# Kernel optimization log

Hardware: AMD Instinct MI355X
Metric: run time of the kernel (lower is better)

The kernel has to match this reference:

```python
import jax, jax.numpy as jnp
import numpy as np

B, D_IN, D_OUT, N_SUBNET, G = 16384, 512, 512, 8, 2


def setup_inputs() -> dict:
    key = jax.random.key(0)
    k_x, k_g, k_w = jax.random.split(key, 3)
    x = jax.random.normal(k_x, (B, D_IN), dtype=jnp.float32)
    groups = jax.random.randint(k_g, (B, G), 0, N_SUBNET, dtype=jnp.int32)
    # per-expert Dense params (the 'subnets')
    W = jax.random.normal(k_w, (N_SUBNET, D_IN, D_OUT), dtype=jnp.float32) * (1.0 / np.sqrt(D_IN))
    b = jnp.zeros((N_SUBNET, D_OUT), dtype=jnp.float32)
    return {"x": x, "groups": groups, "W": W, "b": b}


def reference(x, groups, W, b):
    """SubnetGate: one-hot gated dispatch to per-group subnets + combine.

    Faithful math: gates = one_hot(groups[:, group_col], n_subnet);
    out = sum_e gates[:, e] * subnet_e(x). Since gates are one-hot the
    combine selects exactly one expert output per row (gate weight 1.0).
    """
    group_col = 0
    n_subnet = W.shape[0]
    idx_group = groups[:, group_col]                     # [B]
    gates = jax.nn.one_hot(idx_group, n_subnet, dtype=x.dtype)  # [B, E]
    # run every expert on the full batch (dense reference for the
    # gather-compute-scatter kernel), then gate-combine
    expert_out = jnp.einsum("bi,eio->beo", x, W) + b[None, :, :]  # [B, E, O]
    out = jnp.einsum("be,beo->bo", gates, expert_out)             # [B, O]
    return out
```

## Files before the change

### kernel.cpp

```cpp
#include <hip/hip_runtime.h>
#include <hip/hip_bf16.h>


#define NROWS   16384
#define KDIM    512
#define NDIM    512
#define NEXP    8
#define BM      128
#define BN      128
#define BK      64
#define NT_PER  4
#define KT_PER  8
#define TILE_ELEMS (BN * BK)
#define WS_ROWLIST_OFF 4096
#define WS_WT_OFF      (4096 + NEXP * NROWS * 4)

typedef __bf16        bf16x8 __attribute__((ext_vector_type(8)));
typedef float         f32x4  __attribute__((ext_vector_type(4)));
typedef unsigned int  u32x4  __attribute__((ext_vector_type(4)));

__device__ __forceinline__ unsigned int f2bf_u(float f) {
    unsigned int u = __builtin_bit_cast(unsigned int, f);
    return (u + 0x7FFFu + ((u >> 16) & 1u)) >> 16;
}

__device__ __forceinline__ void gl_lds16(const void* g, void* l) {
    __builtin_amdgcn_global_load_lds(
        (const __attribute__((address_space(1))) unsigned int*)g,
        (__attribute__((address_space(3))) unsigned int*)l, 16, 0, 0);
}

__global__ void zero_kernel(int* __restrict__ gcnt) {
    if (threadIdx.x < NEXP) gcnt[threadIdx.x] = 0;
}

__global__ void prep_kernel(const float* __restrict__ W,
                            const int* __restrict__ groups,
                            int* __restrict__ gcnt,
                            int* __restrict__ rowlist,
                            unsigned short* __restrict__ Wtile) {
    __shared__ __align__(16) unsigned short tl[TILE_ELEMS];
    __shared__ int lcnt[NEXP];
    __shared__ int lbase[NEXP];
    const int bid = blockIdx.x;
    const int tid = threadIdx.x;

    if (bid < 256) {
        const int e  = bid >> 5;
        const int nt = (bid >> 3) & 3;
        const int kt = bid & 7;
        const float* Wb = W + (size_t)e * (KDIM * NDIM);
        #pragma unroll
        for (int i = 0; i < 4; ++i) {
            int f = i * 256 + tid;
            int n = f & 127;
            int g = f >> 7;
            int col = nt * BN + n;
            unsigned int p[4];
            #pragma unroll
            for (int jj = 0; jj < 4; ++jj) {
                int k0 = kt * BK + g * 8 + jj * 2;
                unsigned int lo = f2bf_u(Wb[(size_t)k0 * NDIM + col]);
                unsigned int hi = f2bf_u(Wb[(size_t)(k0 + 1) * NDIM + col]);
                p[jj] = lo | (hi << 16);
            }
            *(u32x4*)&tl[n * 64 + (g ^ (n & 7)) * 8] = *(const u32x4*)p;
        }
        __syncthreads();
        unsigned short* dst = Wtile + (size_t)bid * TILE_ELEMS;
        #pragma unroll
        for (int i = 0; i < 4; ++i) {
            int off = (i * 256 + tid) * 8;
            *(u32x4*)&dst[off] = *(const u32x4*)&tl[off];
        }
    } else {
        const int base = (bid - 256) * 256;
        if (tid < NEXP) lcnt[tid] = 0;
        __syncthreads();
        int r = base + tid;
        int e = groups[r * 2];
        int pos = atomicAdd(&lcnt[e], 1);
        __syncthreads();
        if (tid < NEXP) lbase[tid] = atomicAdd(&gcnt[tid], lcnt[tid]);
        __syncthreads();
        rowlist[e * NROWS + lbase[e] + pos] = r;
    }
}

__global__ __launch_bounds__(256, 2)
void gemm_kernel(const float* __restrict__ x,
                 const int* __restrict__ counts,
                 const int* __restrict__ rowlist,
                 const unsigned short* __restrict__ Wtile,
                 const float* __restrict__ bias,
                 float* __restrict__ out) {
    __shared__ __align__(16) unsigned short Asm[BM * 72];
    __shared__ __align__(16) unsigned short Bsm[TILE_ELEMS];

    const int bid = blockIdx.x;
    const int e   = bid >> 9;
    const int mt  = (bid >> 2) & 127;
    const int nt  = bid & 3;
    const int cnt = counts[e];
    const int rb  = mt * BM;
    if (rb >= cnt) return;
    int m_valid = cnt - rb;
    if (m_valid > BM) m_valid = BM;
    const int* rl = rowlist + e * NROWS + rb;

    const int tid = threadIdx.x;
    const int w   = tid >> 6;
    const int ln  = tid & 63;
    const int q   = ln >> 4;
    const int l15 = ln & 15;
    const int wm  = (w >> 1) * 64;
    const int wn  = (w & 1) * 64;

    const float* srcp[4];
    #pragma unroll
    for (int i = 0; i < 4; ++i) {
        int f = i * 256 + tid;
        int m = f >> 3;
        int g = f & 7;
        srcp[i] = (m < m_valid) ? (x + (size_t)rl[m] * KDIM + g * 8) : nullptr;
    }

    const unsigned short* wt =
        Wtile + (size_t)((e * NT_PER + nt) * KT_PER) * TILE_ELEMS;

    f32x4 acc[4][4];
    #pragma unroll
    for (int mi = 0; mi < 4; ++mi)
        #pragma unroll
        for (int ni = 0; ni < 4; ++ni)
            acc[mi][ni] = (f32x4){0.f, 0.f, 0.f, 0.f};

    for (int kt = 0; kt < KT_PER; ++kt) {
        const unsigned short* wsrc = wt + (size_t)kt * TILE_ELEMS;
        #pragma unroll
        for (int i = 0; i < 4; ++i) {
            int off = (i * 256 + tid) * 8;
            gl_lds16(wsrc + off, &Bsm[off]);
        }
        #pragma unroll
        for (int i = 0; i < 4; ++i) {
            int f = i * 256 + tid;
            int m = f >> 3;
            int g = f & 7;
            u32x4 pack = {0u, 0u, 0u, 0u};
            if (srcp[i]) {
                const float* s = srcp[i] + kt * BK;
                f32x4 f0 = *(const f32x4*)s;
                f32x4 f1 = *(const f32x4*)(s + 4);
                pack.x = f2bf_u(f0.x) | (f2bf_u(f0.y) << 16);
                pack.y = f2bf_u(f0.z) | (f2bf_u(f0.w) << 16);
                pack.z = f2bf_u(f1.x) | (f2bf_u(f1.y) << 16);
                pack.w = f2bf_u(f1.z) | (f2bf_u(f1.w) << 16);
            }
            *(u32x4*)&Asm[m * 72 + g * 8] = pack;
        }
        __syncthreads();
        #pragma unroll
        for (int ks = 0; ks < 2; ++ks) {
            const int g = ks * 4 + q;
            bf16x8 af[4], bf[4];
            #pragma unroll
            for (int mi = 0; mi < 4; ++mi)
                af[mi] = *(const bf16x8*)&Asm[(wm + mi * 16 + l15) * 72 + g * 8];
            #pragma unroll
            for (int ni = 0; ni < 4; ++ni) {
                int n = wn + ni * 16 + l15;
                bf[ni] = *(const bf16x8*)&Bsm[n * 64 + (g ^ (n & 7)) * 8];
            }
            #pragma unroll
            for (int mi = 0; mi < 4; ++mi)
                #pragma unroll
                for (int ni = 0; ni < 4; ++ni)
                    acc[mi][ni] = __builtin_amdgcn_mfma_f32_16x16x32_bf16(
                        af[mi], bf[ni], acc[mi][ni], 0, 0, 0);
        }
        __syncthreads();
    }

    int growv[16];
    #pragma unroll
    for (int mi = 0; mi < 4; ++mi)
        #pragma unroll
        for (int r = 0; r < 4; ++r) {
            int rloc = wm + mi * 16 + q * 4 + r;
            growv[mi * 4 + r] = (rloc < m_valid) ? rl[rloc] : -1;
        }
    const int ncol0 = nt * BN + wn;
    #pragma unroll
    for (int ni = 0; ni < 4; ++ni) {
        int col = ncol0 + ni * 16 + l15;
        float bv = bias[e * NDIM + col];
        #pragma unroll
        for (int mi = 0; mi < 4; ++mi)
            #pragma unroll
            for (int r = 0; r < 4; ++r) {
                int gr = growv[mi * 4 + r];
                if (gr >= 0) out[(size_t)gr * NDIM + col] = acc[mi][ni][r] + bv;
            }
    }
}

extern "C" void kernel_launch(void* const* d_in, const int* in_sizes, int n_in,
                              void* d_out, int out_size, void* d_ws, size_t ws_size,
                              hipStream_t stream) {
    const float* x      = (const float*)d_in[0];
    const int*   groups = (const int*)d_in[1];
    const float* W      = (const float*)d_in[2];
    const float* b      = (const float*)d_in[3];
    float*       out    = (float*)d_out;

    char* ws = (char*)d_ws;
    int*            counts  = (int*)ws;
    int*            rowlist = (int*)(ws + WS_ROWLIST_OFF);
    unsigned short* Wtile   = (unsigned short*)(ws + WS_WT_OFF);

    zero_kernel<<<1, 64, 0, stream>>>(counts);
    prep_kernel<<<320, 256, 0, stream>>>(W, groups, counts, rowlist, Wtile);
    gemm_kernel<<<4096, 256, 0, stream>>>(x, counts, rowlist, Wtile, b, out);
}
```

Before: 122.5 us.

## Restructure grouped GEMM with register-direct A, double-buffered B, smaller M tile

The GEMM kernel now loads activations straight from global memory into registers in MFMA fragment layout, dropping the A shared-memory stage. It double-buffers the weight tile in LDS with prefetch of the next K slice, and halves BM to 64 so each wave owns 16 rows. Occupancy rises to 4 blocks per CU, blocks are interleaved across experts, and output writes use nontemporal stores. The weight prep is split over 4x more blocks, and the zero kernel is replaced with a memset. The trade-off is that weight tiles are reused across fewer rows, and the register-direct A loads are less coalesced.

After: 128.2 us. 4.6% more time.

```diff
diff --git a/kernel.cpp b/kernel.cpp
--- a/kernel.cpp
+++ b/kernel.cpp
@@ -6,7 +6,7 @@
 #define KDIM    512
 #define NDIM    512
 #define NEXP    8
-#define BM      128
+#define BM      64
 #define BN      128
 #define BK      64
 #define NT_PER  4
@@ -30,8 +30,13 @@
         (__attribute__((address_space(3))) unsigned int*)l, 16, 0, 0);
 }
 
-__global__ void zero_kernel(int* __restrict__ gcnt) {
-    if (threadIdx.x < NEXP) gcnt[threadIdx.x] = 0;
+__device__ __forceinline__ bf16x8 pack_bf8(f32x4 lo, f32x4 hi) {
+    u32x4 w;
+    w.x = f2bf_u(lo.x) | (f2bf_u(lo.y) << 16);
+    w.y = f2bf_u(lo.z) | (f2bf_u(lo.w) << 16);
+    w.z = f2bf_u(hi.x) | (f2bf_u(hi.y) << 16);
+    w.w = f2bf_u(hi.z) | (f2bf_u(hi.w) << 16);
+    return __builtin_bit_cast(bf16x8, w);
 }
 
 __global__ void prep_kernel(const float* __restrict__ W,
@@ -39,46 +44,42 @@
                             int* __restrict__ gcnt,
                             int* __restrict__ rowlist,
                             unsigned short* __restrict__ Wtile) {
-    __shared__ __align__(16) unsigned short tl[TILE_ELEMS];
+    __shared__ __align__(16) unsigned short tl4[32 * 64];
     __shared__ int lcnt[NEXP];
     __shared__ int lbase[NEXP];
     const int bid = blockIdx.x;
     const int tid = threadIdx.x;
 
-    if (bid < 256) {
-        const int e  = bid >> 5;
-        const int nt = (bid >> 3) & 3;
-        const int kt = bid & 7;
+    if (bid < 1024) {
+        const int tile = bid >> 2;
+        const int qq   = bid & 3;
+        const int e  = tile >> 5;
+        const int nt = (tile >> 3) & 3;
+        const int kt = tile & 7;
         const float* Wb = W + (size_t)e * (KDIM * NDIM);
-        #pragma unroll
-        for (int i = 0; i < 4; ++i) {
-            int f = i * 256 + tid;
-            int n = f & 127;
-            int g = f >> 7;
-            int col = nt * BN + n;
-            unsigned int p[4];
-            #pragma unroll
-            for (int jj = 0; jj < 4; ++jj) {
-                int k0 = kt * BK + g * 8 + jj * 2;
-                unsigned int lo = f2bf_u(Wb[(size_t)k0 * NDIM + col]);
-                unsigned int hi = f2bf_u(Wb[(size_t)(k0 + 1) * NDIM + col]);
-                p[jj] = lo | (hi << 16);
-            }
-            *(u32x4*)&tl[n * 64 + (g ^ (n & 7)) * 8] = *(const u32x4*)p;
-        }
-        __syncthreads();
-        unsigned short* dst = Wtile + (size_t)bid * TILE_ELEMS;
-        #pragma unroll
-        for (int i = 0; i < 4; ++i) {
-            int off = (i * 256 + tid) * 8;
-            *(u32x4*)&dst[off] = *(const u32x4*)&tl[off];
-        }
+
+        const int n   = qq * 32 + (tid & 31);
+        const int g   = tid >> 5;
+        const int col = nt * BN + n;
+        unsigned int p[4];
+        #pragma unroll
+        for (int jj = 0; jj < 4; ++jj) {
+            int k0 = kt * BK + g * 8 + jj * 2;
+            unsigned int lo = f2bf_u(Wb[(size_t)k0 * NDIM + col]);
+            unsigned int hi = f2bf_u(Wb[(size_t)(k0 + 1) * NDIM + col]);
+            p[jj] = lo | (hi << 16);
+        }
+        *(u32x4*)&tl4[(n & 31) * 64 + (g ^ (n & 7)) * 8] = *(const u32x4*)p;
+        __syncthreads();
+        unsigned short* dst = Wtile + (size_t)tile * TILE_ELEMS
+                                    + ((size_t)qq * 256 + tid) * 8;
+        *(u32x4*)dst = *(const u32x4*)&tl4[tid * 8];
     } else {
-        const int base = (bid - 256) * 256;
+        const int base = (bid - 1024) * 256;
         if (tid < NEXP) lcnt[tid] = 0;
         __syncthreads();
         int r = base + tid;
-        int e = groups[r * 2];
+        int e = groups[r * 2] & 7;
         int pos = atomicAdd(&lcnt[e], 1);
         __syncthreads();
         if (tid < NEXP) lbase[tid] = atomicAdd(&gcnt[tid], lcnt[tid]);
@@ -87,20 +88,20 @@
     }
 }
 
-__global__ __launch_bounds__(256, 2)
+__global__ __launch_bounds__(256, 4)
 void gemm_kernel(const float* __restrict__ x,
                  const int* __restrict__ counts,
                  const int* __restrict__ rowlist,
                  const unsigned short* __restrict__ Wtile,
                  const float* __restrict__ bias,
                  float* __restrict__ out) {
-    __shared__ __align__(16) unsigned short Asm[BM * 72];
-    __shared__ __align__(16) unsigned short Bsm[TILE_ELEMS];
+    __shared__ __align__(16) unsigned short Bsm[2][TILE_ELEMS];
 
     const int bid = blockIdx.x;
-    const int e   = bid >> 9;
-    const int mt  = (bid >> 2) & 127;
-    const int nt  = bid & 3;
+    const int e   = bid & 7;
+    const int j   = bid >> 3;
+    const int nt  = j & 3;
+    const int mt  = j >> 2;
     const int cnt = counts[e];
     const int rb  = mt * BM;
     if (rb >= cnt) return;
@@ -113,95 +114,79 @@
     const int ln  = tid & 63;
     const int q   = ln >> 4;
     const int l15 = ln & 15;
-    const int wm  = (w >> 1) * 64;
-    const int wn  = (w & 1) * 64;
-
-    const float* srcp[4];
-    #pragma unroll
-    for (int i = 0; i < 4; ++i) {
-        int f = i * 256 + tid;
-        int m = f >> 3;
-        int g = f & 7;
-        srcp[i] = (m < m_valid) ? (x + (size_t)rl[m] * KDIM + g * 8) : nullptr;
-    }
+
+    const int am = w * 16 + l15;
+    const float* aptr = x + (size_t)rl[(am < m_valid) ? am : 0] * KDIM + q * 8;
 
     const unsigned short* wt =
         Wtile + (size_t)((e * NT_PER + nt) * KT_PER) * TILE_ELEMS;
 
-    f32x4 acc[4][4];
-    #pragma unroll
-    for (int mi = 0; mi < 4; ++mi)
-        #pragma unroll
-        for (int ni = 0; ni < 4; ++ni)
-            acc[mi][ni] = (f32x4){0.f, 0.f, 0.f, 0.f};
+    f32x4 a0, a1, a2, a3;
+    f32x4 acc[8];
+    #pragma unroll
+    for (int ni = 0; ni < 8; ++ni) acc[ni] = (f32x4){0.f, 0.f, 0.f, 0.f};
+
+    #pragma unroll
+    for (int i = 0; i < 4; ++i) {
+        int off = (i * 256 + tid) * 8;
+        gl_lds16(wt + off, &Bsm[0][off]);
+    }
+    a0 = *(const f32x4*)aptr;
+    a1 = *(const f32x4*)(aptr + 4);
+    a2 = *(const f32x4*)(aptr + 32);
+    a3 = *(const f32x4*)(aptr + 36);
 
     for (int kt = 0; kt < KT_PER; ++kt) {
-        const unsigned short* wsrc = wt + (size_t)kt * TILE_ELEMS;
-        #pragma unroll
-        for (int i = 0; i < 4; ++i) {
-            int off = (i * 256 + tid) * 8;
-            gl_lds16(wsrc + off, &Bsm[off]);
-        }
-        #pragma unroll
-        for (int i = 0; i < 4; ++i) {
-            int f = i * 256 + tid;
-            int m = f >> 3;
-            int g = f & 7;
-            u32x4 pack = {0u, 0u, 0u, 0u};
-            if (srcp[i]) {
-                const float* s = srcp[i] + kt * BK;
-                f32x4 f0 = *(const f32x4*)s;
-                f32x4 f1 = *(const f32x4*)(s + 4);
-                pack.x = f2bf_u(f0.x) | (f2bf_u(f0.y) << 16);
-                pack.y = f2bf_u(f0.z) | (f2bf_u(f0.w) << 16);
-                pack.z = f2bf_u(f1.x) | (f2bf_u(f1.y) << 16);
-                pack.w = f2bf_u(f1.z) | (f2bf_u(f1.w) << 16);
+        __syncthreads();
+        if (kt < KT_PER - 1) {
+            const unsigned short* src = wt + (size_t)(kt + 1) * TILE_ELEMS;
+            unsigned short* dstl = Bsm[(kt + 1) & 1];
+            #pragma unroll
+            for (int i = 0; i < 4; ++i) {
+                int off = (i * 256 + tid) * 8;
+                gl_lds16(src + off, dstl + off);
             }
-            *(u32x4*)&Asm[m * 72 + g * 8] = pack;
-        }
-        __syncthreads();
-        #pragma unroll
-        for (int ks = 0; ks < 2; ++ks) {
-            const int g = ks * 4 + q;
-            bf16x8 af[4], bf[4];
-            #pragma unroll
-            for (int mi = 0; mi < 4; ++mi)
-                af[mi] = *(const bf16x8*)&Asm[(wm + mi * 16 + l15) * 72 + g * 8];
-            #pragma unroll
-            for (int ni = 0; ni < 4; ++ni) {
-                int n = wn + ni * 16 + l15;
-                bf[ni] = *(const bf16x8*)&Bsm[n * 64 + (g ^ (n & 7)) * 8];
-            }
-            #pragma unroll
-            for (int mi = 0; mi < 4; ++mi)
-                #pragma unroll
-                for (int ni = 0; ni < 4; ++ni)
-                    acc[mi][ni] = __builtin_amdgcn_mfma_f32_16x16x32_bf16(
-                        af[mi], bf[ni], acc[mi][ni], 0, 0, 0);
-        }
-        __syncthreads();
-    }
-
-    int growv[16];
-    #pragma unroll
-    for (int mi = 0; mi < 4; ++mi)
-        #pragma unroll
-        for (int r = 0; r < 4; ++r) {
-            int rloc = wm + mi * 16 + q * 4 + r;
-            growv[mi * 4 + r] = (rloc < m_valid) ? rl[rloc] : -1;
-        }
-    const int ncol0 = nt * BN + wn;
-    #pragma unroll
-    for (int ni = 0; ni < 4; ++ni) {
+        }
+        bf16x8 af0 = pack_bf8(a0, a1);
+        bf16x8 af1 = pack_bf8(a2, a3);
+        if (kt < KT_PER - 1) {
+            const float* s = aptr + (kt + 1) * BK;
+            a0 = *(const f32x4*)s;
+            a1 = *(const f32x4*)(s + 4);
+            a2 = *(const f32x4*)(s + 32);
+            a3 = *(const f32x4*)(s + 36);
+        }
+        const unsigned short* bcur = Bsm[kt & 1];
+        #pragma unroll
+        for (int ni = 0; ni < 8; ++ni) {
+            int n = ni * 16 + l15;
+            bf16x8 b0 = *(const bf16x8*)&bcur[n * 64 + (q ^ (n & 7)) * 8];
+            acc[ni] = __builtin_amdgcn_mfma_f32_16x16x32_bf16(af0, b0, acc[ni], 0, 0, 0);
+        }
+        #pragma unroll
+        for (int ni = 0; ni < 8; ++ni) {
+            int n = ni * 16 + l15;
+            bf16x8 b1 = *(const bf16x8*)&bcur[n * 64 + ((4 + q) ^ (n & 7)) * 8];
+            acc[ni] = __builtin_amdgcn_mfma_f32_16x16x32_bf16(af1, b1, acc[ni], 0, 0, 0);
+        }
+    }
+
+    int grow[4];
+    #pragma unroll
+    for (int r = 0; r < 4; ++r) {
+        int mloc = w * 16 + q * 4 + r;
+        grow[r] = (mloc < m_valid) ? rl[mloc] : -1;
+    }
+    const int ncol0 = nt * BN;
+    #pragma unroll
+    for (int ni = 0; ni < 8; ++ni) {
         int col = ncol0 + ni * 16 + l15;
         float bv = bias[e * NDIM + col];
         #pragma unroll
-        for (int mi = 0; mi < 4; ++mi)
-            #pragma unroll
-            for (int r = 0; r < 4; ++r) {
-                int gr = growv[mi * 4 + r];
-                if (gr >= 0) out[(size_t)gr * NDIM + col] = acc[mi][ni][r] + bv;
-            }
+        for (int r = 0; r < 4; ++r)
+            if (grow[r] >= 0)
+                __builtin_nontemporal_store(acc[ni][r] + bv,
+                                            &out[(size_t)grow[r] * NDIM + col]);
     }
 }
 
@@ -219,7 +204,7 @@
     int*            rowlist = (int*)(ws + WS_ROWLIST_OFF);
     unsigned short* Wtile   = (unsigned short*)(ws + WS_WT_OFF);
 
-    zero_kernel<<<1, 64, 0, stream>>>(counts);
-    prep_kernel<<<320, 256, 0, stream>>>(W, groups, counts, rowlist, Wtile);
-    gemm_kernel<<<4096, 256, 0, stream>>>(x, counts, rowlist, Wtile, b, out);
-}
+    hipMemsetAsync(counts, 0, NEXP * sizeof(int), stream);
+    prep_kernel<<<1088, 256, 0, stream>>>(W, groups, counts, rowlist, Wtile);
+    gemm_kernel<<<8192, 256, 0, stream>>>(x, counts, rowlist, Wtile, b, out);
+}
```
